# Optimization experiments

Measured on AMD Instinct MI355X. Metric: run time of the kernel, lower is better.

The kernel has to match this reference:

```python
import jax, jax.numpy as jnp
import numpy as np

L, N, K = 12, 4096, 8   # tree levels, padded nodes per level, max children
V, E, H = 50000, 300, 300


def setup_inputs() -> dict:
    key = jax.random.key(0)
    ks = jax.random.split(key, 24)
    word_ids = jax.random.randint(ks[0], (L, N), 0, V)
    child_idx = jax.random.randint(ks[1], (L, N, K), 0, N)
    child_mask = (jax.random.uniform(ks[2], (L, N, K)) < 0.7).astype(jnp.float32)
    child_mask = child_mask.at[0].set(0.0)  # level 0 nodes are leaves (no children)
    s_e = 1.0 / np.sqrt(E)
    s_h = 1.0 / np.sqrt(H)
    inp = {
        'word_ids': word_ids,
        'child_idx': child_idx,
        'child_mask': child_mask,
        'embedding': jax.random.normal(ks[3], (V, E), jnp.float32),
    }
    for t, g in enumerate(['i', 'f', 'o', 'u']):
        inp['w_' + g] = jax.random.normal(ks[4 + 4 * t], (H, E), jnp.float32) * s_e
        inp['b_w' + g] = jax.random.normal(ks[5 + 4 * t], (H,), jnp.float32) * s_e
        inp['u_' + g] = jax.random.normal(ks[6 + 4 * t], (H, H), jnp.float32) * s_h
        inp['b_u' + g] = jax.random.normal(ks[7 + 4 * t], (H,), jnp.float32) * s_h
    return inp


def _lin(x, W, b):
    # torch nn.Linear: x @ W.T + b
    return jnp.matmul(x, W.T) + b


def reference(word_ids, child_idx, child_mask, embedding,
              w_i, b_wi, u_i, b_ui, w_f, b_wf, u_f, b_uf,
              w_o, b_wo, u_o, b_uo, w_u, b_wu, u_u, b_uu):
    n = word_ids.shape[1]
    h_dim = w_i.shape[0]
    dt = embedding.dtype

    def step(carry, level):
        h_prev, c_prev = carry           # [N, H] from previous tree level
        wids, cidx, cmask = level        # [N], [N, K], [N, K]
        x = embedding[wids]              # [N, E]
        h_k = h_prev[cidx]               # [N, K, H] variable-arity child gather
        c_k = c_prev[cidx]               # [N, K, H]
        m = cmask[..., None]             # [N, K, 1]
        # per-child forget gate: sigmoid(w_f(x_j) + u_f(h_k))
        f = jax.nn.sigmoid(_lin(x, w_f, b_wf)[:, None, :] + _lin(h_k, u_f, b_uf))
        h_tilde = jnp.sum(m * h_k, axis=1)        # child-sum of hidden states
        sum_c = jnp.sum(m * f * c_k, axis=1)      # gated child cell sum
        i = jax.nn.sigmoid(_lin(x, w_i, b_wi) + _lin(h_tilde, u_i, b_ui))
        o = jax.nn.sigmoid(_lin(x, w_o, b_wo) + _lin(h_tilde, u_o, b_uo))
        u = jnp.tanh(_lin(x, w_u, b_wu) + _lin(h_tilde, u_u, b_uu))
        c = i * u + sum_c
        h = o * jnp.tanh(c)
        return (h, c), None

    init = (jnp.zeros((n, h_dim), dt), jnp.zeros((n, h_dim), dt))
    (h, c), _ = jax.lax.scan(step, init, (word_ids, child_idx, child_mask))
    return h, c
```

## Files before the change

kernel.cpp:

```cpp
#include <hip/hip_runtime.h>
#include <cmath>
#include <cstdint>


#define NN    4096
#define HH    300
#define KK    8
#define LVLS  12
#define KP    320
#define MTOT  49152

typedef __bf16  bf16x8 __attribute__((ext_vector_type(8)));
typedef float   f32x4  __attribute__((ext_vector_type(4)));

#define GAS __attribute__((address_space(1)))
#define LAS __attribute__((address_space(3)))

__device__ __forceinline__ float sigmoidf_(float x) {
    return 1.0f / (1.0f + expf(-x));
}
__device__ __forceinline__ ushort f2bf(float f) {
    union { float f; uint32_t u; } v; v.f = f;
    return (ushort)((v.u + 0x7fffu + ((v.u >> 16) & 1u)) >> 16);
}
__device__ __forceinline__ float bf2f(ushort u) {
    union { uint32_t u; float f; } v; v.u = ((uint32_t)u) << 16;
    return v.f;
}

__global__ __launch_bounds__(256)
void pack_and_stage(
    const float* __restrict__ wi, const float* __restrict__ bwi,
    const float* __restrict__ ui, const float* __restrict__ bui,
    const float* __restrict__ wf, const float* __restrict__ bwf,
    const float* __restrict__ uf, const float* __restrict__ buf_,
    const float* __restrict__ wo, const float* __restrict__ bwo,
    const float* __restrict__ uo, const float* __restrict__ buo,
    const float* __restrict__ wu, const float* __restrict__ bwu,
    const float* __restrict__ uu, const float* __restrict__ buu,
    ushort* __restrict__ WfP, ushort* __restrict__ Uf, ushort* __restrict__ Wz,
    float* __restrict__ BZ, float* __restrict__ Bwf, float* __restrict__ BUF,
    const int* __restrict__ word_ids, const float* __restrict__ emb,
    ushort* __restrict__ X)
{
    const int b = blockIdx.x;
    if (b >= 3207) {
        int idx = (b - 3207) * 256 + threadIdx.x;
        int kb = idx / MTOT, row = idx % MTOT;
        const int k0 = kb * 8;
        ushort o[8];
        if (kb < 37) {
            const float4* p = reinterpret_cast<const float4*>(
                emb + (size_t)word_ids[row] * 300 + k0);
            float4 v0 = p[0], v1 = p[1];
            o[0] = f2bf(v0.x); o[1] = f2bf(v0.y); o[2] = f2bf(v0.z); o[3] = f2bf(v0.w);
            o[4] = f2bf(v1.x); o[5] = f2bf(v1.y); o[6] = f2bf(v1.z); o[7] = f2bf(v1.w);
        } else if (kb == 37) {
            const float4 v0 = *reinterpret_cast<const float4*>(
                emb + (size_t)word_ids[row] * 300 + k0);
            o[0] = f2bf(v0.x); o[1] = f2bf(v0.y); o[2] = f2bf(v0.z); o[3] = f2bf(v0.w);
            o[4] = o[5] = o[6] = o[7] = 0;
        } else {
            o[0] = o[1] = o[2] = o[3] = o[4] = o[5] = o[6] = o[7] = 0;
        }
        ushort* dst = X + ((size_t)kb * MTOT + row) * 8;
        ushort4 a; a.x = o[0]; a.y = o[1]; a.z = o[2]; a.w = o[3];
        ushort4 c; c.x = o[4]; c.y = o[5]; c.z = o[6]; c.w = o[7];
        *reinterpret_cast<ushort4*>(dst)     = a;
        *reinterpret_cast<ushort4*>(dst + 4) = c;
        return;
    }
    int t = b * 256 + threadIdx.x;
    if (t < 102400) {
        int r = t / KP, k = t % KP;
        WfP[((size_t)(k >> 3) * KP + r) * 8 + (k & 7)] =
            f2bf((r < 300 && k < 300) ? wf[r * 300 + k] : 0.f);
    } else if (t < 204800) {
        int x = t - 102400, r = x / KP, k = x % KP;
        Uf[x] = f2bf((r < 300 && k < 300) ? uf[r * 300 + k] : 0.f);
    } else if (t < 819200) {
        int x = t - 204800;
        int g = x / 204800, rem = x % 204800;
        int r = rem / 640, k = rem % 640;
        const float* W = (g == 0) ? wi : (g == 1) ? wo : wu;
        const float* U = (g == 0) ? ui : (g == 1) ? uo : uu;
        float v = 0.f;
        if (r < 300) {
            if (k < 320) { if (k < 300) v = W[r * 300 + k]; }
            else         { int kk = k - 320; if (kk < 300) v = U[r * 300 + kk]; }
        }
        Wz[(((size_t)g * 80 + (k >> 3)) * KP + r) * 8 + (k & 7)] = f2bf(v);
    } else if (t < 820160) {
        int x = t - 819200, g = x / KP, r = x % KP;
        const float* bw = (g == 0) ? bwi : (g == 1) ? bwo : bwu;
        const float* bu = (g == 0) ? bui : (g == 1) ? buo : buu;
        BZ[x] = (r < 300) ? bw[r] + bu[r] : 0.f;
    } else if (t < 820480) {
        int r = t - 820160;
        Bwf[r] = (r < 300) ? bwf[r] : 0.f;
    } else if (t < 820800) {
        int r = t - 820480;
        BUF[r] = (r < 300) ? buf_[r] : 0.f;
    }
}

__global__ __launch_bounds__(256)
void wxf_all_kernel(const ushort* __restrict__ Xp, const ushort* __restrict__ WfPp,
                    const float* __restrict__ Bwf, ushort* __restrict__ WXFall)
{
    __shared__ __attribute__((aligned(16))) ushort As[2][8][128][8];
    __shared__ __attribute__((aligned(16))) ushort Bs[2][8][64][8];

    const int b  = blockIdx.x;
    const int bj = (b % 8) * 240 + b / 8;
    const int m0 = (bj / 5) * 128, n0 = (bj % 5) * 64;

    const int t = threadIdx.x, l = t & 63, w = t >> 6;
    const int m_off = (w >> 1) * 64, n_off = (w & 1) * 32;
    const int kq = l >> 4, lr = l & 15;

    f32x4 acc[4][2] = {};

    auto STAGE = [&](int buf, int s) {
        #pragma unroll
        for (int c = 0; c < 4; ++c) {
            const int slot = t + 256 * c;
            const int kb = slot >> 7, row = slot & 127;
            const ushort* src = Xp + ((size_t)(s * 8 + kb) * MTOT + m0 + row) * 8;
            __builtin_amdgcn_global_load_lds((const GAS void*)src,
                (LAS void*)&As[buf][kb][row][0], 16, 0, 0);
        }
        #pragma unroll
        for (int c = 0; c < 2; ++c) {
            const int slot = t + 256 * c;
            const int kb = slot >> 6, row = slot & 63;
            const ushort* src = WfPp + ((size_t)(s * 8 + kb) * KP + n0 + row) * 8;
            __builtin_amdgcn_global_load_lds((const GAS void*)src,
                (LAS void*)&Bs[buf][kb][row][0], 16, 0, 0);
        }
    };
    auto COMPUTE = [&](int buf) {
        #pragma unroll
        for (int kk = 0; kk < 2; ++kk) {
            const int kc = kk * 4 + kq;
            bf16x8 af[4], bfr[2];
            #pragma unroll
            for (int mi = 0; mi < 4; ++mi)
                af[mi] = *reinterpret_cast<const bf16x8*>(
                    &As[buf][kc][m_off + mi * 16 + lr][0]);
            #pragma unroll
            for (int ni = 0; ni < 2; ++ni)
                bfr[ni] = *reinterpret_cast<const bf16x8*>(
                    &Bs[buf][kc][n_off + ni * 16 + lr][0]);
            #pragma unroll
            for (int mi = 0; mi < 4; ++mi)
                #pragma unroll
                for (int ni = 0; ni < 2; ++ni)
                    acc[mi][ni] = __builtin_amdgcn_mfma_f32_16x16x32_bf16(
                        af[mi], bfr[ni], acc[mi][ni], 0, 0, 0);
        }
    };

    STAGE(0, 0);
    #pragma unroll
    for (int s = 0; s < 4; ++s) {
        STAGE((s + 1) & 1, s + 1);
        asm volatile("s_waitcnt vmcnt(6)" ::: "memory");
        __builtin_amdgcn_s_barrier();
        COMPUTE(s & 1);
        __builtin_amdgcn_s_barrier();
    }
    asm volatile("s_waitcnt vmcnt(0)" ::: "memory");
    __builtin_amdgcn_s_barrier();
    COMPUTE(0);

    const int col = l & 15, r0 = (l >> 4) * 4;
    #pragma unroll
    for (int mi = 0; mi < 4; ++mi) {
        #pragma unroll
        for (int ni = 0; ni < 2; ++ni) {
            const int gn = n0 + n_off + ni * 16 + col;
            const float bb = Bwf[gn];
            #pragma unroll
            for (int r = 0; r < 4; ++r) {
                const int gm = m0 + m_off + mi * 16 + r0 + r;
                WXFall[(size_t)gm * KP + gn] = f2bf(acc[mi][ni][r] + bb);
            }
        }
    }
}

__device__ __forceinline__ int swz640(int b) { return (b % 8) * 80 + b / 8; }

__global__ __launch_bounds__(128)
void fp_kernel(const ushort* __restrict__ Hbf, const ushort* __restrict__ Uf,
               const float* __restrict__ BUF, ushort* __restrict__ FP)
{
    const int bj = swz640((int)blockIdx.x);
    const int m0 = (bj / 10) * 64, n0 = (bj % 10) * 32;
    const int t = threadIdx.x, w = t >> 6, l = t & 63;
    const int kq = l >> 4, lr = l & 15, m_off = w * 32;

    f32x4 acc[2][2] = {};
    #pragma unroll
    for (int s = 0; s < 10; ++s) {
        const int kc = s * 4 + kq;
        bf16x8 af[2], bfr[2];
        #pragma unroll
        for (int mi = 0; mi < 2; ++mi)
            af[mi] = *reinterpret_cast<const bf16x8*>(
                Hbf + (size_t)(m0 + m_off + mi * 16 + lr) * KP + (size_t)kc * 8);
        #pragma unroll
        for (int ni = 0; ni < 2; ++ni)
            bfr[ni] = *reinterpret_cast<const bf16x8*>(
                Uf + (size_t)(n0 + ni * 16 + lr) * KP + (size_t)kc * 8);
        #pragma unroll
        for (int mi = 0; mi < 2; ++mi)
            #pragma unroll
            for (int ni = 0; ni < 2; ++ni)
                acc[mi][ni] = __builtin_amdgcn_mfma_f32_16x16x32_bf16(
                    af[mi], bfr[ni], acc[mi][ni], 0, 0, 0);
    }

    const int col = l & 15, r0 = (l >> 4) * 4;
    #pragma unroll
    for (int mi = 0; mi < 2; ++mi) {
        #pragma unroll
        for (int ni = 0; ni < 2; ++ni) {
            const int gn = n0 + ni * 16 + col;
            const float bb = BUF[gn];
            #pragma unroll
            for (int r = 0; r < 4; ++r) {
                const int gm = m0 + m_off + mi * 16 + r0 + r;
                FP[(size_t)gm * KP + gn] = f2bf(acc[mi][ni][r] + bb);
            }
        }
    }
}

__global__ __launch_bounds__(320)
void reduce_kernel(const ushort* __restrict__ Hbf, const float* __restrict__ Cst,
                   const ushort* __restrict__ FP, const ushort* __restrict__ WXF,
                   const int* __restrict__ cidx, const float* __restrict__ cmask,
                   ushort* __restrict__ HTp, float* __restrict__ SC)
{
    const int x = threadIdx.x;
    const int ty = threadIdx.y;
    const int n = blockIdx.x * 4 + ty;
    __shared__ int   ch[4][KK];
    __shared__ float mk[4][KK];
    if (x < KK) {
        ch[ty][x] = cidx[n * KK + x];
        mk[ty][x] = cmask[n * KK + x];
    }
    __syncthreads();
    if (x >= 75) {
        ushort4 z; z.x = z.y = z.z = z.w = 0;
        const int pi = x - 75;
        const int kb = 37 + ((pi + 1) >> 1);
        const int off = ((pi & 1) ^ 1) * 4;
        *reinterpret_cast<ushort4*>(
            HTp + ((size_t)kb * NN + n) * 8 + off) = z;
        return;
    }
    const int h = x * 4;

    ushort4 hu[KK]; ushort4 fu[KK]; float4 cv[KK];
    #pragma unroll
    for (int k = 0; k < KK; ++k) {
        const size_t cr = (size_t)ch[ty][k];
        hu[k] = *reinterpret_cast<const ushort4*>(&Hbf[cr * KP + h]);
        fu[k] = *reinterpret_cast<const ushort4*>(&FP [cr * KP + h]);
        cv[k] = *reinterpret_cast<const float4*>(&Cst[cr * HH + h]);
    }

    ushort4 wxu = *reinterpret_cast<const ushort4*>(&WXF[(size_t)n * KP + h]);
    const float wx0 = bf2f(wxu.x), wx1 = bf2f(wxu.y),
                wx2 = bf2f(wxu.z), wx3 = bf2f(wxu.w);
    float ht0 = 0.f, ht1 = 0.f, ht2 = 0.f, ht3 = 0.f;
    float sc0 = 0.f, sc1 = 0.f, sc2 = 0.f, sc3 = 0.f;

    #pragma unroll
    for (int k = 0; k < KK; ++k) {
        const float m = mk[ty][k];
        if (m != 0.f) {
            ht0 += m * bf2f(hu[k].x); ht1 += m * bf2f(hu[k].y);
            ht2 += m * bf2f(hu[k].z); ht3 += m * bf2f(hu[k].w);
            sc0 += m * sigmoidf_(wx0 + bf2f(fu[k].x)) * cv[k].x;
            sc1 += m * sigmoidf_(wx1 + bf2f(fu[k].y)) * cv[k].y;
            sc2 += m * sigmoidf_(wx2 + bf2f(fu[k].z)) * cv[k].z;
            sc3 += m * sigmoidf_(wx3 + bf2f(fu[k].w)) * cv[k].w;
        }
    }
    ushort4 ho; ho.x = f2bf(ht0); ho.y = f2bf(ht1); ho.z = f2bf(ht2); ho.w = f2bf(ht3);
    *reinterpret_cast<ushort4*>(
        HTp + ((size_t)(x >> 1) * NN + n) * 8 + (x & 1) * 4) = ho;
    float4 so; so.x = sc0; so.y = sc1; so.z = sc2; so.w = sc3;
    *reinterpret_cast<float4*>(&SC[(size_t)n * KP + h]) = so;
}

__global__ __launch_bounds__(256)
void zgemm(const ushort* __restrict__ Xlev, const ushort* __restrict__ HTp,
           const ushort* __restrict__ Wzp, const float* __restrict__ BZ,
           const float* __restrict__ SC,
           float* __restrict__ cdst, ushort* __restrict__ Hb,
           float* __restrict__ hdst)
{
    __shared__ __attribute__((aligned(16))) ushort As[2][8][64][8];
    __shared__ __attribute__((aligned(16))) ushort Bs[2][3][8][32][8];

    const int b  = blockIdx.x;
    const int bj = (b % 8) * 80 + b / 8;
    const int m0 = (bj / 10) * 64, j0 = (bj % 10) * 32;

    const int t = threadIdx.x, w = t >> 6, l = t & 63;
    const int kq = l >> 4, lr = l & 15;
    const int m_off = (w >> 1) * 32, j_off = (w & 1) * 16;

    f32x4 acc[3][2] = {};

    auto STAGE = [&](int buf, int s) {
        #pragma unroll
        for (int c = 0; c < 2; ++c) {
            const int slot = t + 256 * c;
            const int kb = slot >> 6, row = slot & 63;
            const int kcg = s * 8 + kb;
            const ushort* src = (kcg < 40)
                ? (Xlev + ((size_t)kcg * MTOT + m0 + row) * 8)
                : (HTp  + ((size_t)(kcg - 40) * NN + m0 + row) * 8);
            __builtin_amdgcn_global_load_lds((const GAS void*)src,
                (LAS void*)&As[buf][kb][row][0], 16, 0, 0);
        }
        #pragma unroll
        for (int c = 0; c < 3; ++c) {
            const int slot = t + 256 * c;
            const int g = slot >> 8, rem = slot & 255;
            const int kb = rem >> 5, row = rem & 31;
            const ushort* src = Wzp +
                (((size_t)g * 80 + s * 8 + kb) * KP + j0 + row) * 8;
            __builtin_amdgcn_global_load_lds((const GAS void*)src,
                (LAS void*)&Bs[buf][g][kb][row][0], 16, 0, 0);
        }
    };
    auto COMPUTE = [&](int buf) {
        #pragma unroll
        for (int kk = 0; kk < 2; ++kk) {
            const int kc = kk * 4 + kq;
            bf16x8 af[2], bfr[3];
            #pragma unroll
            for (int mi = 0; mi < 2; ++mi)
                af[mi] = *reinterpret_cast<const bf16x8*>(
                    &As[buf][kc][m_off + mi * 16 + lr][0]);
            #pragma unroll
            for (int g = 0; g < 3; ++g)
                bfr[g] = *reinterpret_cast<const bf16x8*>(
                    &Bs[buf][g][kc][j_off + lr][0]);
            #pragma unroll
            for (int g = 0; g < 3; ++g)
                #pragma unroll
                for (int mi = 0; mi < 2; ++mi)
                    acc[g][mi] = __builtin_amdgcn_mfma_f32_16x16x32_bf16(
                        af[mi], bfr[g], acc[g][mi], 0, 0, 0);
        }
    };

    STAGE(0, 0);
    #pragma unroll
    for (int s = 0; s < 9; ++s) {
        STAGE((s + 1) & 1, s + 1);
        asm volatile("s_waitcnt vmcnt(5)" ::: "memory");
        __builtin_amdgcn_s_barrier();
        COMPUTE(s & 1);
        __builtin_amdgcn_s_barrier();
    }
    asm volatile("s_waitcnt vmcnt(0)" ::: "memory");
    __builtin_amdgcn_s_barrier();
    COMPUTE(1);

    const int col = l & 15, r0 = (l >> 4) * 4;
    const int gn = j0 + j_off + col;
    if (gn < 300) {
        const float bi_ = BZ[gn], bo_ = BZ[KP + gn], bu_ = BZ[2 * KP + gn];
        #pragma unroll
        for (int mi = 0; mi < 2; ++mi) {
            #pragma unroll
            for (int r = 0; r < 4; ++r) {
                const int gm = m0 + m_off + mi * 16 + r0 + r;
                const float sc = SC[(size_t)gm * KP + gn];
                const float ig = sigmoidf_(acc[0][mi][r] + bi_);
                const float og = sigmoidf_(acc[1][mi][r] + bo_);
                const float ug = tanhf   (acc[2][mi][r] + bu_);
                const float c  = ig * ug + sc;
                const float hv = og * tanhf(c);
                cdst[(size_t)gm * HH + gn] = c;
                Hb  [(size_t)gm * KP + gn] = f2bf(hv);
                if (hdst) hdst[(size_t)gm * HH + gn] = hv;
            }
        }
    }
}

extern "C" void kernel_launch(void* const* d_in, const int* in_sizes, int n_in,
                              void* d_out, int out_size, void* d_ws, size_t ws_size,
                              hipStream_t stream)
{
    const int*   word_ids   = (const int*)  d_in[0];
    const int*   child_idx  = (const int*)  d_in[1];
    const float* child_mask = (const float*)d_in[2];
    const float* emb        = (const float*)d_in[3];
    const float* w_i  = (const float*)d_in[4];  const float* b_wi = (const float*)d_in[5];
    const float* u_i  = (const float*)d_in[6];  const float* b_ui = (const float*)d_in[7];
    const float* w_f  = (const float*)d_in[8];  const float* b_wf = (const float*)d_in[9];
    const float* u_f  = (const float*)d_in[10]; const float* b_uf = (const float*)d_in[11];
    const float* w_o  = (const float*)d_in[12]; const float* b_wo = (const float*)d_in[13];
    const float* u_o  = (const float*)d_in[14]; const float* b_uo = (const float*)d_in[15];
    const float* w_u  = (const float*)d_in[16]; const float* b_wu = (const float*)d_in[17];
    const float* u_u  = (const float*)d_in[18]; const float* b_uu = (const float*)d_in[19];

    uint8_t* ws = (uint8_t*)d_ws;
    size_t off = 0;
    auto alloc = [&](size_t bytes) {
        uint8_t* p = ws + off;
        off += (bytes + 255) & ~(size_t)255;
        return p;
    };
    ushort* WfP   = (ushort*)alloc((size_t)KP * KP * 2);
    ushort* Uf    = (ushort*)alloc((size_t)KP * KP * 2);
    ushort* Wz    = (ushort*)alloc((size_t)3 * KP * 640 * 2);
    ushort* Xall  = (ushort*)alloc((size_t)40 * MTOT * 8 * 2);
    ushort* WXFall= (ushort*)alloc((size_t)LVLS * NN * KP * 2);
    ushort* FPbf  = (ushort*)alloc((size_t)NN * KP * 2);
    ushort* HTbf  = (ushort*)alloc((size_t)40 * NN * 8 * 2);
    ushort* Hbf   = (ushort*)alloc((size_t)NN * KP * 2);
    float*  SCb   = (float*) alloc((size_t)NN * KP * 4);
    float*  C0    = (float*) alloc((size_t)NN * HH * 4);
    float*  BZ    = (float*) alloc(3 * KP * 4);
    float*  Bwf   = (float*) alloc(KP * 4);
    float*  BUFb  = (float*) alloc(KP * 4);

    pack_and_stage<<<10887, 256, 0, stream>>>(
        w_i, b_wi, u_i, b_ui, w_f, b_wf, u_f, b_uf,
        w_o, b_wo, u_o, b_uo, w_u, b_wu, u_u, b_uu,
        WfP, Uf, Wz, BZ, Bwf, BUFb,
        word_ids, emb, Xall);
    wxf_all_kernel<<<1920, 256, 0, stream>>>(Xall, WfP, Bwf, WXFall);

    float* h_final = (float*)d_out;
    float* c_final = (float*)d_out + (size_t)NN * HH;

    for (int lev = 0; lev < LVLS; ++lev) {
        const int*    cidx  = child_idx  + (size_t)lev * NN * KK;
        const float*  cmask = child_mask + (size_t)lev * NN * KK;
        const ushort* Xlev  = Xall + (size_t)lev * NN * 8;
        const ushort* WXFlev= WXFall + (size_t)lev * NN * KP;
        const bool last = (lev == LVLS - 1);
        float* cdst = last ? c_final : C0;
        float* hdst = last ? h_final : nullptr;

        if (lev > 0)
            fp_kernel<<<640, 128, 0, stream>>>(Hbf, Uf, BUFb, FPbf);
        reduce_kernel<<<1024, dim3(80, 4), 0, stream>>>(
            Hbf, C0, FPbf, WXFlev, cidx, cmask, HTbf, SCb);
        zgemm<<<640, 256, 0, stream>>>(
            Xlev, HTbf, Wz, BZ, SCb, cdst, Hbf, hdst);
    }
}
```

Measured before the change: 513.1 us.

## Hoist all input-side gate projections into one batched GEMM before the level loop

The W·x projections for the i, o and u gates now join the forget-gate projection in a single large GEMM over all levels, done once before the sequential tree loop. The per-level zgemm then only multiplies the child hidden sum by U, halving its K, and reads the precomputed x-terms in its epilogue. fp_kernel is rewritten to use LDS double-buffering with global_load_lds from a K-blocked copy of h that zgemm also writes. The trade is a much larger up-front GEMM and a big bf16 ZW buffer (49152x1280), plus strided gather reads of the x-terms in the epilogue.

```diff
diff --git a/kernel.cpp b/kernel.cpp
--- a/kernel.cpp
+++ b/kernel.cpp
@@ -9,6 +9,7 @@
 #define LVLS  12
 #define KP    320
 #define MTOT  49152
+#define NW    1280
 
 typedef __bf16  bf16x8 __attribute__((ext_vector_type(8)));
 typedef float   f32x4  __attribute__((ext_vector_type(4)));
@@ -38,14 +39,15 @@
     const float* __restrict__ uo, const float* __restrict__ buo,
     const float* __restrict__ wu, const float* __restrict__ bwu,
     const float* __restrict__ uu, const float* __restrict__ buu,
-    ushort* __restrict__ WfP, ushort* __restrict__ Uf, ushort* __restrict__ Wz,
+    ushort* __restrict__ W4, ushort* __restrict__ Ufp, ushort* __restrict__ WzU,
     float* __restrict__ BZ, float* __restrict__ Bwf, float* __restrict__ BUF,
+    ushort* __restrict__ Hk,
     const int* __restrict__ word_ids, const float* __restrict__ emb,
     ushort* __restrict__ X)
 {
     const int b = blockIdx.x;
-    if (b >= 3207) {
-        int idx = (b - 3207) * 256 + threadIdx.x;
+    if (b >= 3527) {
+        int idx = (b - 3527) * 256 + threadIdx.x;
         int kb = idx / MTOT, row = idx % MTOT;
         const int k0 = kb * 8;
         ushort o[8];
@@ -71,25 +73,24 @@
         return;
     }
     int t = b * 256 + threadIdx.x;
-    if (t < 102400) {
-        int r = t / KP, k = t % KP;
-        WfP[((size_t)(k >> 3) * KP + r) * 8 + (k & 7)] =
-            f2bf((r < 300 && k < 300) ? wf[r * 300 + k] : 0.f);
-    } else if (t < 204800) {
-        int x = t - 102400, r = x / KP, k = x % KP;
-        Uf[x] = f2bf((r < 300 && k < 300) ? uf[r * 300 + k] : 0.f);
+    if (t < 409600) {
+        int gate = t / 102400, rem = t % 102400;
+        int r = rem / 320, k = rem % 320;
+        const float* W = (gate == 0) ? wf : (gate == 1) ? wi
+                       : (gate == 2) ? wo : wu;
+        float v = (r < 300 && k < 300) ? W[r * 300 + k] : 0.f;
+        W4[((size_t)(k >> 3) * NW + gate * 320 + r) * 8 + (k & 7)] = f2bf(v);
+    } else if (t < 512000) {
+        int x = t - 409600, r = x / 320, k = x % 320;
+        Ufp[((size_t)(k >> 3) * KP + r) * 8 + (k & 7)] =
+            f2bf((r < 300 && k < 300) ? uf[r * 300 + k] : 0.f);
     } else if (t < 819200) {
-        int x = t - 204800;
-        int g = x / 204800, rem = x % 204800;
-        int r = rem / 640, k = rem % 640;
-        const float* W = (g == 0) ? wi : (g == 1) ? wo : wu;
+        int x = t - 512000;
+        int g = x / 102400, rem = x % 102400;
+        int r = rem / 320, k = rem % 320;
         const float* U = (g == 0) ? ui : (g == 1) ? uo : uu;
-        float v = 0.f;
-        if (r < 300) {
-            if (k < 320) { if (k < 300) v = W[r * 300 + k]; }
-            else         { int kk = k - 320; if (kk < 300) v = U[r * 300 + kk]; }
-        }
-        Wz[(((size_t)g * 80 + (k >> 3)) * KP + r) * 8 + (k & 7)] = f2bf(v);
+        WzU[(((size_t)g * 40 + (k >> 3)) * KP + r) * 8 + (k & 7)] =
+            f2bf((r < 300 && k < 300) ? U[r * 300 + k] : 0.f);
     } else if (t < 820160) {
         int x = t - 819200, g = x / KP, r = x % KP;
         const float* bw = (g == 0) ? bwi : (g == 1) ? bwo : bwu;
@@ -101,19 +102,24 @@
     } else if (t < 820800) {
         int r = t - 820480;
         BUF[r] = (r < 300) ? buf_[r] : 0.f;
+    } else if (t < 902720) {
+        int x = t - 820800;
+        int row = x / 20, pe = x % 20;
+        int k = 300 + pe;
+        Hk[((size_t)(k >> 3) * NN + row) * 8 + (k & 7)] = 0;
     }
 }
 
 __global__ __launch_bounds__(256)
-void wxf_all_kernel(const ushort* __restrict__ Xp, const ushort* __restrict__ WfPp,
-                    const float* __restrict__ Bwf, ushort* __restrict__ WXFall)
+void zx_all_kernel(const ushort* __restrict__ Xp, const ushort* __restrict__ W4,
+                   const float* __restrict__ Bwf, ushort* __restrict__ ZW)
 {
     __shared__ __attribute__((aligned(16))) ushort As[2][8][128][8];
     __shared__ __attribute__((aligned(16))) ushort Bs[2][8][64][8];
 
     const int b  = blockIdx.x;
-    const int bj = (b % 8) * 240 + b / 8;
-    const int m0 = (bj / 5) * 128, n0 = (bj % 5) * 64;
+    const int bj = (b % 8) * 960 + b / 8;
+    const int m0 = (bj / 20) * 128, n0 = (bj % 20) * 64;
 
     const int t = threadIdx.x, l = t & 63, w = t >> 6;
     const int m_off = (w >> 1) * 64, n_off = (w & 1) * 32;
@@ -134,7 +140,7 @@
         for (int c = 0; c < 2; ++c) {
             const int slot = t + 256 * c;
             const int kb = slot >> 6, row = slot & 63;
-            const ushort* src = WfPp + ((size_t)(s * 8 + kb) * KP + n0 + row) * 8;
+            const ushort* src = W4 + ((size_t)(s * 8 + kb) * NW + n0 + row) * 8;
             __builtin_amdgcn_global_load_lds((const GAS void*)src,
                 (LAS void*)&Bs[buf][kb][row][0], 16, 0, 0);
         }
@@ -180,67 +186,96 @@
         #pragma unroll
         for (int ni = 0; ni < 2; ++ni) {
             const int gn = n0 + n_off + ni * 16 + col;
-            const float bb = Bwf[gn];
+            const float bb = (gn < 320) ? Bwf[gn] : 0.f;
             #pragma unroll
             for (int r = 0; r < 4; ++r) {
                 const int gm = m0 + m_off + mi * 16 + r0 + r;
-                WXFall[(size_t)gm * KP + gn] = f2bf(acc[mi][ni][r] + bb);
+                ZW[(size_t)gm * NW + gn] = f2bf(acc[mi][ni][r] + bb);
             }
         }
     }
 }
 
-__device__ __forceinline__ int swz640(int b) { return (b % 8) * 80 + b / 8; }
-
-__global__ __launch_bounds__(128)
-void fp_kernel(const ushort* __restrict__ Hbf, const ushort* __restrict__ Uf,
-               const float* __restrict__ BUF, ushort* __restrict__ FP)
+__global__ __launch_bounds__(256)
+void fp_kernel(const ushort* __restrict__ Hk, const ushort* __restrict__ Ufp,
+               const float* __restrict__ BUFb, ushort* __restrict__ FP)
 {
-    const int bj = swz640((int)blockIdx.x);
-    const int m0 = (bj / 10) * 64, n0 = (bj % 10) * 32;
+    __shared__ __attribute__((aligned(16))) ushort As[2][8][64][8];
+    __shared__ __attribute__((aligned(16))) ushort Bs[2][8][32][8];
+
+    const int b  = blockIdx.x;
+    const int bj = (b % 8) * 80 + b / 8;
+    const int m0 = (bj / 10) * 64, j0 = (bj % 10) * 32;
+
     const int t = threadIdx.x, w = t >> 6, l = t & 63;
-    const int kq = l >> 4, lr = l & 15, m_off = w * 32;
-
-    f32x4 acc[2][2] = {};
+    const int kq = l >> 4, lr = l & 15;
+    const int m_off = (w >> 1) * 32, j_off = (w & 1) * 16;
+
+    f32x4 acc[2] = {};
+
+    auto STAGE = [&](int buf, int s) {
+        #pragma unroll
+        for (int c = 0; c < 2; ++c) {
+            const int slot = t + 256 * c;
+            const int kb = slot >> 6, row = slot & 63;
+            const ushort* src = Hk + ((size_t)(s * 8 + kb) * NN + m0 + row) * 8;
+            __builtin_amdgcn_global_load_lds((const GAS void*)src,
+                (LAS void*)&As[buf][kb][row][0], 16, 0, 0);
+        }
+        {
+            const int kb = t >> 5, row = t & 31;
+            const ushort* src = Ufp + ((size_t)(s * 8 + kb) * KP + j0 + row) * 8;
+            __builtin_amdgcn_global_load_lds((const GAS void*)src,
+                (LAS void*)&Bs[buf][kb][row][0], 16, 0, 0);
+        }
+    };
+    auto COMPUTE = [&](int buf) {
+        #pragma unroll
+        for (int kk = 0; kk < 2; ++kk) {
+            const int kc = kk * 4 + kq;
+            bf16x8 af[2], bf;
+            #pragma unroll
+            for (int mi = 0; mi < 2; ++mi)
+                af[mi] = *reinterpret_cast<const bf16x8*>(
+                    &As[buf][kc][m_off + mi * 16 + lr][0]);
+            bf = *reinterpret_cast<const bf16x8*>(
+                    &Bs[buf][kc][j_off + lr][0]);
+            #pragma unroll
+            for (int mi = 0; mi < 2; ++mi)
+                acc[mi] = __builtin_amdgcn_mfma_f32_16x16x32_bf16(
+                    af[mi], bf, acc[mi], 0, 0, 0);
+        }
+    };
+
+    STAGE(0, 0);
     #pragma unroll
-    for (int s = 0; s < 10; ++s) {
-        const int kc = s * 4 + kq;
-        bf16x8 af[2], bfr[2];
+    for (int s = 0; s < 4; ++s) {
+        STAGE((s + 1) & 1, s + 1);
+        asm volatile("s_waitcnt vmcnt(3)" ::: "memory");
+        __builtin_amdgcn_s_barrier();
+        COMPUTE(s & 1);
+        __builtin_amdgcn_s_barrier();
+    }
+    asm volatile("s_waitcnt vmcnt(0)" ::: "memory");
+    __builtin_amdgcn_s_barrier();
+    COMPUTE(0);
+
+    const int col = l & 15, r0 = (l >> 4) * 4;
+    const int gn = j0 + j_off + col;
+    if (gn < 300) {
+        const float bb = BUFb[gn];
         #pragma unroll
         for (int mi = 0; mi < 2; ++mi)
-            af[mi] = *reinterpret_cast<const bf16x8*>(
-                Hbf + (size_t)(m0 + m_off + mi * 16 + lr) * KP + (size_t)kc * 8);
-        #pragma unroll
-        for (int ni = 0; ni < 2; ++ni)
-            bfr[ni] = *reinterpret_cast<const bf16x8*>(
-                Uf + (size_t)(n0 + ni * 16 + lr) * KP + (size_t)kc * 8);
-        #pragma unroll
-        for (int mi = 0; mi < 2; ++mi)
-            #pragma unroll
-            for (int ni = 0; ni < 2; ++ni)
-                acc[mi][ni] = __builtin_amdgcn_mfma_f32_16x16x32_bf16(
-                    af[mi], bfr[ni], acc[mi][ni], 0, 0, 0);
-    }
-
-    const int col = l & 15, r0 = (l >> 4) * 4;
-    #pragma unroll
-    for (int mi = 0; mi < 2; ++mi) {
-        #pragma unroll
-        for (int ni = 0; ni < 2; ++ni) {
-            const int gn = n0 + ni * 16 + col;
-            const float bb = BUF[gn];
-            #pragma unroll
-            for (int r = 0; r < 4; ++r) {
-                const int gm = m0 + m_off + mi * 16 + r0 + r;
-                FP[(size_t)gm * KP + gn] = f2bf(acc[mi][ni][r] + bb);
-            }
-        }
+            #pragma unroll
+            for (int r = 0; r < 4; ++r)
+                FP[(size_t)(m0 + m_off + mi * 16 + r0 + r) * KP + gn] =
+                    f2bf(acc[mi][r] + bb);
     }
 }
 
 __global__ __launch_bounds__(320)
 void reduce_kernel(const ushort* __restrict__ Hbf, const float* __restrict__ Cst,
-                   const ushort* __restrict__ FP, const ushort* __restrict__ WXF,
+                   const ushort* __restrict__ FP, const ushort* __restrict__ ZWlev,
                    const int* __restrict__ cidx, const float* __restrict__ cmask,
                    ushort* __restrict__ HTp, float* __restrict__ SC)
 {
@@ -274,7 +309,7 @@
         cv[k] = *reinterpret_cast<const float4*>(&Cst[cr * HH + h]);
     }
 
-    ushort4 wxu = *reinterpret_cast<const ushort4*>(&WXF[(size_t)n * KP + h]);
+    ushort4 wxu = *reinterpret_cast<const ushort4*>(&ZWlev[(size_t)n * NW + h]);
     const float wx0 = bf2f(wxu.x), wx1 = bf2f(wxu.y),
                 wx2 = bf2f(wxu.z), wx3 = bf2f(wxu.w);
     float ht0 = 0.f, ht1 = 0.f, ht2 = 0.f, ht3 = 0.f;
@@ -300,11 +335,11 @@
 }
 
 __global__ __launch_bounds__(256)
-void zgemm(const ushort* __restrict__ Xlev, const ushort* __restrict__ HTp,
-           const ushort* __restrict__ Wzp, const float* __restrict__ BZ,
-           const float* __restrict__ SC,
+void zgemm(const ushort* __restrict__ HTp, const ushort* __restrict__ WzU,
+           const float* __restrict__ BZ, const float* __restrict__ SC,
+           const ushort* __restrict__ ZXlev,
            float* __restrict__ cdst, ushort* __restrict__ Hb,
-           float* __restrict__ hdst)
+           ushort* __restrict__ Hk, float* __restrict__ hdst)
 {
     __shared__ __attribute__((aligned(16))) ushort As[2][8][64][8];
     __shared__ __attribute__((aligned(16))) ushort Bs[2][3][8][32][8];
@@ -324,10 +359,7 @@
         for (int c = 0; c < 2; ++c) {
             const int slot = t + 256 * c;
             const int kb = slot >> 6, row = slot & 63;
-            const int kcg = s * 8 + kb;
-            const ushort* src = (kcg < 40)
-                ? (Xlev + ((size_t)kcg * MTOT + m0 + row) * 8)
-                : (HTp  + ((size_t)(kcg - 40) * NN + m0 + row) * 8);
+            const ushort* src = HTp + ((size_t)(s * 8 + kb) * NN + m0 + row) * 8;
             __builtin_amdgcn_global_load_lds((const GAS void*)src,
                 (LAS void*)&As[buf][kb][row][0], 16, 0, 0);
         }
@@ -336,8 +368,8 @@
             const int slot = t + 256 * c;
             const int g = slot >> 8, rem = slot & 255;
             const int kb = rem >> 5, row = rem & 31;
-            const ushort* src = Wzp +
-                (((size_t)g * 80 + s * 8 + kb) * KP + j0 + row) * 8;
+            const ushort* src = WzU +
+                (((size_t)g * 40 + s * 8 + kb) * KP + j0 + row) * 8;
             __builtin_amdgcn_global_load_lds((const GAS void*)src,
                 (LAS void*)&Bs[buf][g][kb][row][0], 16, 0, 0);
         }
@@ -366,7 +398,7 @@
 
     STAGE(0, 0);
     #pragma unroll
-    for (int s = 0; s < 9; ++s) {
+    for (int s = 0; s < 4; ++s) {
         STAGE((s + 1) & 1, s + 1);
         asm volatile("s_waitcnt vmcnt(5)" ::: "memory");
         __builtin_amdgcn_s_barrier();
@@ -375,7 +407,7 @@
     }
     asm volatile("s_waitcnt vmcnt(0)" ::: "memory");
     __builtin_amdgcn_s_barrier();
-    COMPUTE(1);
+    COMPUTE(0);
 
     const int col = l & 15, r0 = (l >> 4) * 4;
     const int gn = j0 + j_off + col;
@@ -386,14 +418,20 @@
             #pragma unroll
             for (int r = 0; r < 4; ++r) {
                 const int gm = m0 + m_off + mi * 16 + r0 + r;
+                const size_t zb = (size_t)gm * NW + 320 + gn;
+                const float zi = bf2f(ZXlev[zb]);
+                const float zo = bf2f(ZXlev[zb + 320]);
+                const float zu = bf2f(ZXlev[zb + 640]);
                 const float sc = SC[(size_t)gm * KP + gn];
-                const float ig = sigmoidf_(acc[0][mi][r] + bi_);
-                const float og = sigmoidf_(acc[1][mi][r] + bo_);
-                const float ug = tanhf   (acc[2][mi][r] + bu_);
+                const float ig = sigmoidf_(acc[0][mi][r] + zi + bi_);
+                const float og = sigmoidf_(acc[1][mi][r] + zo + bo_);
+                const float ug = tanhf   (acc[2][mi][r] + zu + bu_);
                 const float c  = ig * ug + sc;
                 const float hv = og * tanhf(c);
                 cdst[(size_t)gm * HH + gn] = c;
-                Hb  [(size_t)gm * KP + gn] = f2bf(hv);
+                const ushort hb = f2bf(hv);
+                Hb[(size_t)gm * KP + gn] = hb;
+                Hk[((size_t)(gn >> 3) * NN + gm) * 8 + (gn & 7)] = hb;
                 if (hdst) hdst[(size_t)gm * HH + gn] = hv;
             }
         }
@@ -424,26 +462,27 @@
         off += (bytes + 255) & ~(size_t)255;
         return p;
     };
-    ushort* WfP   = (ushort*)alloc((size_t)KP * KP * 2);
-    ushort* Uf    = (ushort*)alloc((size_t)KP * KP * 2);
-    ushort* Wz    = (ushort*)alloc((size_t)3 * KP * 640 * 2);
+    ushort* W4    = (ushort*)alloc((size_t)40 * NW * 8 * 2);
+    ushort* Ufp   = (ushort*)alloc((size_t)40 * KP * 8 * 2);
+    ushort* WzU   = (ushort*)alloc((size_t)3 * 40 * KP * 8 * 2);
     ushort* Xall  = (ushort*)alloc((size_t)40 * MTOT * 8 * 2);
-    ushort* WXFall= (ushort*)alloc((size_t)LVLS * NN * KP * 2);
+    ushort* ZW    = (ushort*)alloc((size_t)MTOT * NW * 2);
     ushort* FPbf  = (ushort*)alloc((size_t)NN * KP * 2);
-    ushort* HTbf  = (ushort*)alloc((size_t)40 * NN * 8 * 2);
+    ushort* HTp   = (ushort*)alloc((size_t)40 * NN * 8 * 2);
     ushort* Hbf   = (ushort*)alloc((size_t)NN * KP * 2);
+    ushort* Hk    = (ushort*)alloc((size_t)40 * NN * 8 * 2);
     float*  SCb   = (float*) alloc((size_t)NN * KP * 4);
     float*  C0    = (float*) alloc((size_t)NN * HH * 4);
     float*  BZ    = (float*) alloc(3 * KP * 4);
     float*  Bwf   = (float*) alloc(KP * 4);
     float*  BUFb  = (float*) alloc(KP * 4);
 
-    pack_and_stage<<<10887, 256, 0, stream>>>(
+    pack_and_stage<<<11207, 256, 0, stream>>>(
         w_i, b_wi, u_i, b_ui, w_f, b_wf, u_f, b_uf,
         w_o, b_wo, u_o, b_uo, w_u, b_wu, u_u, b_uu,
-        WfP, Uf, Wz, BZ, Bwf, BUFb,
+        W4, Ufp, WzU, BZ, Bwf, BUFb, Hk,
         word_ids, emb, Xall);
-    wxf_all_kernel<<<1920, 256, 0, stream>>>(Xall, WfP, Bwf, WXFall);
+    zx_all_kernel<<<7680, 256, 0, stream>>>(Xall, W4, Bwf, ZW);
 
     float* h_final = (float*)d_out;
     float* c_final = (float*)d_out + (size_t)NN * HH;
@@ -451,17 +490,16 @@
     for (int lev = 0; lev < LVLS; ++lev) {
         const int*    cidx  = child_idx  + (size_t)lev * NN * KK;
         const float*  cmask = child_mask + (size_t)lev * NN * KK;
-        const ushort* Xlev  = Xall + (size_t)lev * NN * 8;
-        const ushort* WXFlev= WXFall + (size_t)lev * NN * KP;
+        const ushort* ZWlev = ZW + (size_t)lev * NN * NW;
         const bool last = (lev == LVLS - 1);
         float* cdst = last ? c_final : C0;
         float* hdst = last ? h_final : nullptr;
 
         if (lev > 0)
-            fp_kernel<<<640, 128, 0, stream>>>(Hbf, Uf, BUFb, FPbf);
+            fp_kernel<<<640, 256, 0, stream>>>(Hk, Ufp, BUFb, FPbf);
         reduce_kernel<<<1024, dim3(80, 4), 0, stream>>>(
-            Hbf, C0, FPbf, WXFlev, cidx, cmask, HTbf, SCb);
+            Hbf, C0, FPbf, ZWlev, cidx, cmask, HTp, SCb);
         zgemm<<<640, 256, 0, stream>>>(
-            Xlev, HTbf, Wz, BZ, SCb, cdst, Hbf, hdst);
-    }
-}
+            HTp, WzU, BZ, SCb, ZWlev, cdst, Hbf, Hk, hdst);
+    }
+}
```

New measurement: 481.7 us. 6.1% less time.
